# Performance work log

Hardware: AMD Instinct MI355X
Metric: run time of the kernel (lower is better)

The kernel has to match this reference:

```python
import jax, jax.numpy as jnp
from jax import lax
import numpy as np

NEIGHBORS = ((1, 3), (0, 2, 4), (1, 5), (0, 4, 6), (1, 3, 5, 7), (2, 4, 8), (3, 7), (4, 6, 8), (5, 7))
EDGE_SRC = np.array([s for t, ns in enumerate(NEIGHBORS) for s in ns])  # 25 edges
EDGE_DST = np.array([t for t, ns in enumerate(NEIGHBORS) for _ in ns])
NE = len(EDGE_SRC)  # 25
NG, SP = 9, 64      # num_grids, single_plane = 576 // 9
R, C_IN, C_OUT, ROI = 64, 256, 576, 14
GN_GROUPS = 36
EPS = 1e-5


def conv2d(x, w, b, stride, pad):
    y = lax.conv_general_dilated(x, w, (stride, stride), [(pad, pad), (pad, pad)],
                                 dimension_numbers=('NCHW', 'OIHW', 'NCHW'))
    return y + b[None, :, None, None]


def group_norm(x, groups, gamma, beta):
    B, C, H, W = x.shape
    xg = x.reshape(B, groups, -1)
    mu = xg.mean(-1, keepdims=True)
    var = xg.var(-1, keepdims=True)
    xn = ((xg - mu) / jnp.sqrt(var + EPS)).reshape(B, C, H, W)
    return xn * gamma[None, :, None, None] + beta[None, :, None, None]


def edge_conv(inp, dw_w, dw_b, pw_w, pw_b):
    # depthwise 5x5 (groups=SP) then pointwise 1x1
    y = lax.conv_general_dilated(inp, dw_w, (1, 1), [(2, 2), (2, 2)],
                                 dimension_numbers=('NCHW', 'OIHW', 'NCHW'),
                                 feature_group_count=SP) + dw_b[None, :, None, None]
    return jnp.einsum('bchw,oc->bohw', y, pw_w) + pw_b[None, :, None, None]


def deconv_grouped(x, w_t, b, groups):
    # torch ConvTranspose2d(k=4, s=2, p=1, groups) as lhs-dilated conv
    k, s, p = 4, 2, 1
    in_c, out_g = w_t.shape[0], w_t.shape[1]
    in_g = in_c // groups
    w = w_t.reshape(groups, in_g, out_g, k, k).transpose(0, 2, 1, 3, 4).reshape(groups * out_g, in_g, k, k)
    w = jnp.flip(w, (-2, -1))
    y = lax.conv_general_dilated(x, w, (1, 1), [(k - 1 - p, k - 1 - p)] * 2,
                                 lhs_dilation=(s, s),
                                 dimension_numbers=('NCHW', 'OIHW', 'NCHW'),
                                 feature_group_count=groups)
    return y + b[None, :, None, None]


def setup_inputs() -> dict:
    key = jax.random.key(0)
    ks = iter(jax.random.split(key, 32))
    n = lambda shape, s=0.02: jax.random.normal(next(ks), shape, jnp.float32) * s
    inp = {
        'x': jax.random.normal(next(ks), (R, C_IN, ROI, ROI), jnp.float32),
        'convs_w0': n((C_OUT, C_IN, 3, 3)),
        'convs_b0': n((C_OUT,)),
        'convs_w': n((7, C_OUT, C_OUT, 3, 3)),
        'convs_b': n((7, C_OUT)),
        'gn_gamma': jnp.ones((8, C_OUT), jnp.float32),
        'gn_beta': jnp.zeros((8, C_OUT), jnp.float32),
        'fo_dw_w': n((NE, SP, 1, 5, 5), 0.05),
        'fo_dw_b': n((NE, SP)),
        'fo_pw_w': n((NE, SP, SP), 0.05),
        'fo_pw_b': n((NE, SP)),
        'so_dw_w': n((NE, SP, 1, 5, 5), 0.05),
        'so_dw_b': n((NE, SP)),
        'so_pw_w': n((NE, SP, SP), 0.05),
        'so_pw_b': n((NE, SP)),
        'up1_w': n((C_OUT, SP, 4, 4), 0.01),
        'up1_b': jnp.zeros((C_OUT,), jnp.float32),
        'sbn1_gamma': jnp.ones((C_OUT,), jnp.float32),
        'sbn1_beta': jnp.zeros((C_OUT,), jnp.float32),
        'up2_w': n((C_OUT, 1, 4, 4), 0.01),
        'up2_b': jnp.full((NG,), -np.log(0.99 / 0.01), jnp.float32),
    }
    return inp


def reference(x, convs_w0, convs_b0, convs_w, convs_b, gn_gamma, gn_beta,
              fo_dw_w, fo_dw_b, fo_pw_w, fo_pw_b,
              so_dw_w, so_dw_b, so_pw_w, so_pw_b,
              up1_w, up1_b, sbn1_gamma, sbn1_beta, up2_w, up2_b):
    # dense conv stack: stride 2 first, then 7 stride-1 convs (GN + ReLU each)
    h = jax.nn.relu(group_norm(conv2d(x, convs_w0, convs_b0, 2, 1), GN_GROUPS, gn_gamma[0], gn_beta[0]))
    for i in range(7):
        h = jax.nn.relu(group_norm(conv2d(h, convs_w[i], convs_b[i], 1, 1),
                                   GN_GROUPS, gn_gamma[i + 1], gn_beta[i + 1]))
    B, _, Hh, Wh = h.shape  # [B, 576, 7, 7]
    xg = h.reshape(B, NG, SP, Hh, Wh).transpose(1, 0, 2, 3, 4)  # [9, B, 64, 7, 7]
    # first-order message passing over 25 grid edges
    msgs1 = jax.vmap(edge_conv)(xg[EDGE_SRC], fo_dw_w, fo_dw_b, fo_pw_w, fo_pw_b)
    first = xg + jax.ops.segment_sum(msgs1, EDGE_DST, num_segments=NG)
    # second-order message passing (sources are first-order features)
    msgs2 = jax.vmap(edge_conv)(first[EDGE_SRC], so_dw_w, so_dw_b, so_pw_w, so_pw_b)
    second = xg + jax.ops.segment_sum(msgs2, EDGE_DST, num_segments=NG)
    x2 = second.transpose(1, 0, 2, 3, 4).reshape(B, NG * SP, Hh, Wh)

    def head(t):
        t = deconv_grouped(t, up1_w, up1_b, NG)           # [B, 576, 14, 14]
        t = jax.nn.relu(group_norm(t, NG, sbn1_gamma, sbn1_beta))
        return deconv_grouped(t, up2_w, up2_b, NG)        # [B, 9, 28, 28]

    return (head(h), head(x2))
```

## Files before the change

kernel.cpp:

```cpp
#include <hip/hip_runtime.h>
#include <hip/hip_bf16.h>

#define BB 64
#define CIN 256
#define CC 576
#define NGR 9
#define SPC 64
#define HW7 49
#define HW14 196
#define HW28 784

__device__ __constant__ int EDGE_SRC_C[24] = {1,3, 0,2,4, 1,5, 0,4,6, 1,3,5,7, 2,4,8, 3,7, 4,6,8, 5,7};
__device__ __constant__ int EDGE_OFF_C[9]  = {0,2,5,7,10,14,17,19,22};
__device__ __constant__ int EDGE_CNT_C[9]  = {2,3,2,3,4,3,2,3,2};

static __device__ __forceinline__ float bf2f(__hip_bfloat16 v){ return __bfloat162float(v); }
static __device__ __forceinline__ __hip_bfloat16 f2bf(float v){ return __float2bfloat16(v); }
static __device__ __forceinline__ float ldin(const void* p, size_t i, int isbf){
  return isbf ? bf2f(((const __hip_bfloat16*)p)[i]) : ((const float*)p)[i];
}

using bfrag = __attribute__((ext_vector_type(8))) short;
using f32x4 = __attribute__((ext_vector_type(4))) float;

__global__ void detect_kernel(const unsigned short* xs, int* flag) {
  if (threadIdx.x==0 && blockIdx.x==0) {
    int plaus = 0;
    for (int i=0;i<64;i++){
      unsigned short u = xs[2*i];
      int e = (u>>7)&0xFF;
      if (e>=100 && e<=140) plaus++;
    }
    *flag = (plaus >= 40) ? 1 : 0;
  }
}

__global__ __launch_bounds__(256) void xcvt_kernel(
    const void* __restrict__ x, const int* __restrict__ flagp,
    __hip_bfloat16* __restrict__ act0) {
  const int b = blockIdx.x, icb = blockIdx.y, pxb = blockIdx.z, t = threadIdx.x;
  const int isbf = *flagp;
  __shared__ float lds[32][29];
  for (int idx=t; idx<32*28; idx+=256){
    int i = idx/28, j = idx - i*28;
    lds[i][j] = ldin(x, ((size_t)b*CIN + icb*32+i)*HW14 + pxb*28 + j, isbf);
  }
  __syncthreads();
  for (int idx=t; idx<28*32; idx+=256){
    int j = idx >> 5, i = idx & 31;
    act0[((size_t)b*HW14 + pxb*28 + j)*CIN + icb*32 + i] = f2bf(lds[i][j]);
  }
}

__global__ __launch_bounds__(256) void wcvt0_kernel(
    const void* __restrict__ w, const int* __restrict__ flagp,
    __hip_bfloat16* __restrict__ dst) {
  const int oc = blockIdx.x, t = threadIdx.x;
  const int isbf = *flagp;
  __shared__ float lds[2304];
  for (int idx=t; idx<2304; idx+=256)
    lds[idx] = ldin(w, (size_t)oc*2304 + idx, isbf);
  __syncthreads();
  for (int idx=t; idx<2304; idx+=256){
    int koff = idx >> 8, rem = idx & 255;
    int icb = rem >> 5, ici = rem & 31;
    dst[(((size_t)koff*8 + icb)*CC + oc)*32 + ici] = f2bf(lds[rem*9 + koff]);
  }
}

__global__ __launch_bounds__(256) void wcvtL_kernel(
    const void* __restrict__ w, int li, const int* __restrict__ flagp,
    __hip_bfloat16* __restrict__ dst) {
  const int oc = blockIdx.x, t = threadIdx.x;
  const int isbf = *flagp;
  __shared__ float lds[5184];
  for (int idx=t; idx<5184; idx+=256)
    lds[idx] = ldin(w, ((size_t)li*CC + oc)*5184 + idx, isbf);
  __syncthreads();
  for (int idx=t; idx<5184; idx+=256){
    int koff = idx / 576, rem = idx - koff*576;
    int icb = rem >> 5, ici = rem & 31;
    dst[(((size_t)koff*18 + icb)*CC + oc)*32 + ici] = f2bf(lds[rem*9 + koff]);
  }
}

__global__ __launch_bounds__(256) void wcvtAll2_kernel(
    const void* __restrict__ w, const int* __restrict__ flagp,
    __hip_bfloat16* __restrict__ dst_base) {
  const int oc0 = blockIdx.x*2, li = blockIdx.y, t = threadIdx.x;
  const int isbf = *flagp;
  __hip_bfloat16* dst = dst_base + (size_t)li * (9u*18u*576u*32u);
  __shared__ alignas(16) __hip_bfloat16 lds[2*5184];

  if (isbf){
    const unsigned short* ws = (const unsigned short*)w;
    for (int idx=t; idx<1296; idx+=256){
      int ocl = idx/648, j = idx - ocl*648;
      *(bfrag*)(lds + ocl*5184 + j*8) =
        *(const bfrag*)(ws + ((size_t)(li*CC + oc0+ocl))*5184 + j*8);
    }
  } else {
    const float* wf = (const float*)w;
    for (int idx=t; idx<1296; idx+=256){
      int ocl = idx/648, j = idx - ocl*648;
      const float* s = wf + ((size_t)(li*CC + oc0+ocl))*5184 + j*8;
      f32x4 v0 = *(const f32x4*)(s);
      f32x4 v1 = *(const f32x4*)(s+4);
      alignas(16) __hip_bfloat16 tmp[8];
      #pragma unroll
      for (int u=0;u<4;u++){ tmp[u] = f2bf(v0[u]); tmp[4+u] = f2bf(v1[u]); }
      *(bfrag*)(lds + ocl*5184 + j*8) = *(const bfrag*)tmp;
    }
  }
  __syncthreads();

  for (int idx=t; idx<1296; idx+=256){
    int g = idx>>1, ocl = idx&1;
    int koff = g/72, r = g - koff*72;
    int icb = r>>2, q = r&3;
    const __hip_bfloat16* src = lds + ocl*5184;
    alignas(16) __hip_bfloat16 tmp[8];
    #pragma unroll
    for (int u=0;u<8;u++)
      tmp[u] = src[(icb*32 + q*8 + u)*9 + koff];
    *(bfrag*)(dst + (((size_t)koff*18 + icb)*CC + (oc0+ocl))*32 + q*8) =
        *(const bfrag*)tmp;
  }
}

static __device__ __forceinline__ void epilogue_gn(
    float* s_out, float* s_stats, const f32x4 (&acc)[2][2],
    int wm, int wn, int ln, int quad, int t,
    const void* bias, int bias_off,
    const void* gamma, const void* beta, int goff,
    int nbb, int isbf, int b,
    __hip_bfloat16* __restrict__ out)
{
  __syncthreads();
  #pragma unroll
  for (int nf=0; nf<2; nf++){
    int chl = wn*32 + nf*16 + ln;
    float bv = ldin(bias, (size_t)bias_off + nbb + chl, isbf);
    #pragma unroll
    for (int mf=0; mf<2; mf++){
      #pragma unroll
      for (int r=0; r<4; r++){
        int px = wm*32 + mf*16 + quad*4 + r;
        s_out[chl*65 + px] = acc[mf][nf][r] + bv;
      }
    }
  }
  __syncthreads();
  {
    int wv = t >> 6, l = t & 63;
    float s=0.f, ss=0.f;
    for (int j=l; j<784; j+=64){
      int cq = j/49, px = j - cq*49;
      float v = s_out[(wv*16+cq)*65 + px];
      s += v; ss += v*v;
    }
    #pragma unroll
    for (int o=32;o>0;o>>=1){ s+=__shfl_down(s,o); ss+=__shfl_down(ss,o); }
    if (l==0){
      float mean=s/784.f, var=ss/784.f-mean*mean;
      s_stats[wv*2]=mean; s_stats[wv*2+1]=rsqrtf(fmaxf(var,0.f)+1e-5f);
    }
  }
  __syncthreads();
  for (int idx=t; idx<392; idx+=256){
    int px = idx>>3, ck = idx&7;
    alignas(16) __hip_bfloat16 tmp[8];
    #pragma unroll
    for (int u=0;u<8;u++){
      int chl = ck*8+u;
      int gi = chl>>4;
      float ga = ldin(gamma, (size_t)goff + nbb + chl, isbf);
      float be = ldin(beta,  (size_t)goff + nbb + chl, isbf);
      float v = (s_out[chl*65+px]-s_stats[gi*2])*s_stats[gi*2+1]*ga + be;
      tmp[u] = f2bf(fmaxf(v,0.f));
    }
    *(bfrag*)(out + ((size_t)b*64+px)*CC + nbb + ck*8) = *(const bfrag*)tmp;
  }
}

__global__ __launch_bounds__(256) void conv3_v6_kernel(
    const __hip_bfloat16* __restrict__ A,
    const __hip_bfloat16* __restrict__ Wb,
    const void* __restrict__ bias, int bias_off,
    const void* __restrict__ gamma, const void* __restrict__ beta, int goff,
    const int* __restrict__ flagp,
    __hip_bfloat16* __restrict__ out) {
  const int t = threadIdx.x;
  const int l = t & 63, w = t >> 6;
  const int wm = w & 1, wn = (w >> 1) & 1;
  const int ln = l & 15, quad = l >> 4;
  const int b = blockIdx.x, nbb = blockIdx.y*32;
  const int isbf = *flagp;

  __shared__ alignas(16) char smem[14400];
  __shared__ float s_stats[4];
  __hip_bfloat16* sA0 = (__hip_bfloat16*)smem;
  __hip_bfloat16* sA1 = (__hip_bfloat16*)(smem + 7200);
  float* s_out = (float*)smem;

  if (t < 16){
    bfrag z = {0,0,0,0,0,0,0,0};
    __hip_bfloat16* sb = (t<8)? sA0 : sA1;
    *(bfrag*)(sb + 49*72 + (t&7)*8) = z;
  }

  int r0a[9], r1a[9];
  {
    int p0 = wm*32 + ln, p1 = p0+16;
    int y0=p0/7, x0=p0-y0*7, y1=p1/7, x1=p1-y1*7;
    bool v0=p0<49, v1=p1<49;
    #pragma unroll
    for (int koff=0;koff<9;koff++){
      int dy=koff/3-1, dx=koff-(koff/3)*3-1;
      int sy0=y0+dy,sx0=x0+dx, sy1=y1+dy,sx1=x1+dx;
      r0a[koff] = (v0&&sy0>=0&&sy0<7&&sx0>=0&&sx0<7)? sy0*7+sx0 : 49;
      r1a[koff] = (v1&&sy1>=0&&sy1<7&&sx1>=0&&sx1<7)? sy1*7+sx1 : 49;
    }
  }

  f32x4 acc2[2];
  acc2[0] = (f32x4){0.f,0.f,0.f,0.f};
  acc2[1] = (f32x4){0.f,0.f,0.f,0.f};

  const int i0r = t>>3, is8 = (t&7)*8;
  const int i1r = i0r + 32;
  const bool has1 = (t < 136);
  const __hip_bfloat16* Ab = A + (size_t)b*64*CC;

  *(bfrag*)(sA0 + i0r*72 + is8) = *(const bfrag*)(Ab + (size_t)i0r*CC + is8);
  if (has1)
    *(bfrag*)(sA0 + i1r*72 + is8) = *(const bfrag*)(Ab + (size_t)i1r*CC + is8);
  __syncthreads();

  const int nidx = nbb + wn*16 + ln;
  const __hip_bfloat16* wbase = Wb + (size_t)nidx*32 + quad*8;
  for (int c=0; c<9; c++){
    __hip_bfloat16* curb = (c&1)? sA1 : sA0;
    bfrag rs0, rs1;
    const bool pf = (c<8);
    if (pf){
      rs0 = *(const bfrag*)(Ab + (size_t)i0r*CC + (c+1)*64 + is8);
      if (has1) rs1 = *(const bfrag*)(Ab + (size_t)i1r*CC + (c+1)*64 + is8);
    }
    #pragma unroll
    for (int koff=0;koff<9;koff++){
      const int ra0 = r0a[koff]*72 + quad*8;
      const int ra1 = r1a[koff]*72 + quad*8;
      #pragma unroll
      for (int ks=0; ks<2; ks++){
        const __hip_bfloat16* wp = wbase + (size_t)(koff*18 + c*2 + ks)*18432;
        bfrag b0 = *(const bfrag*)(wp);
        bfrag a0 = *(const bfrag*)(curb + ra0 + ks*32);
        bfrag a1 = *(const bfrag*)(curb + ra1 + ks*32);
        acc2[0] = __builtin_amdgcn_mfma_f32_16x16x32_bf16(a0, b0, acc2[0], 0,0,0);
        acc2[1] = __builtin_amdgcn_mfma_f32_16x16x32_bf16(a1, b0, acc2[1], 0,0,0);
      }
    }
    if (pf){
      __hip_bfloat16* nxtb = (c&1)? sA0 : sA1;
      *(bfrag*)(nxtb + i0r*72 + is8) = rs0;
      if (has1) *(bfrag*)(nxtb + i1r*72 + is8) = rs1;
    }
    __syncthreads();
  }

  {
    const int chl = wn*16 + ln;
    float bv = ldin(bias, (size_t)bias_off + nbb + chl, isbf);
    #pragma unroll
    for (int mf=0; mf<2; mf++)
      #pragma unroll
      for (int r=0;r<4;r++){
        int px = wm*32 + mf*16 + quad*4 + r;
        s_out[chl*65 + px] = acc2[mf][r] + bv;
      }
  }
  __syncthreads();
  {
    int wv = t >> 6, l2 = t & 63;
    if (wv < 2){
      float s=0.f, ss=0.f;
      for (int j=l2; j<784; j+=64){
        int cq = j/49, px = j - cq*49;
        float v = s_out[(wv*16+cq)*65 + px];
        s += v; ss += v*v;
      }
      #pragma unroll
      for (int o=32;o>0;o>>=1){ s+=__shfl_down(s,o); ss+=__shfl_down(ss,o); }
      if (l2==0){
        float mean=s/784.f, var=ss/784.f-mean*mean;
        s_stats[wv*2]=mean; s_stats[wv*2+1]=rsqrtf(fmaxf(var,0.f)+1e-5f);
      }
    }
  }
  __syncthreads();
  if (t < 196){
    int px = t>>2, ck = t&3;
    alignas(16) __hip_bfloat16 tmp[8];
    #pragma unroll
    for (int u=0;u<8;u++){
      int chl = ck*8+u;
      int gi = chl>>4;
      float ga = ldin(gamma, (size_t)goff + nbb + chl, isbf);
      float be = ldin(beta,  (size_t)goff + nbb + chl, isbf);
      float v = (s_out[chl*65+px]-s_stats[gi*2])*s_stats[gi*2+1]*ga + be;
      tmp[u] = f2bf(fmaxf(v,0.f));
    }
    *(bfrag*)(out + ((size_t)b*64+px)*CC + nbb + ck*8) = *(const bfrag*)tmp;
  }
}

__global__ __launch_bounds__(256) void conv0_fused_kernel(
    const __hip_bfloat16* __restrict__ A,
    const __hip_bfloat16* __restrict__ Wb,
    const void* __restrict__ bias,
    const void* __restrict__ gamma, const void* __restrict__ beta,
    const int* __restrict__ flagp,
    __hip_bfloat16* __restrict__ out) {
  const int t = threadIdx.x;
  const int l = t & 63, w = t >> 6;
  const int wm = w & 1, wn = w >> 1;
  const int ln = l & 15, quad = l >> 4;
  const int b = blockIdx.x, nbb = blockIdx.y*64;

  __shared__ alignas(16) __hip_bfloat16 sC[197*40];
  __shared__ alignas(16) float s_out_arr[64*65];
  __shared__ float s_stats[8];

  if (t < 4){
    bfrag z = {0,0,0,0,0,0,0,0};
    *(bfrag*)(sC + 196*40 + t*8) = z;
  }

  int yy[2], xx[2]; bool pv[2];
  #pragma unroll
  for (int mf=0; mf<2; mf++){
    int p = wm*32 + mf*16 + ln;
    pv[mf] = p<49; yy[mf]=p/7; xx[mf]=p-yy[mf]*7;
  }

  f32x4 acc[2][2];
  #pragma unroll
  for (int i=0;i<2;i++)
    #pragma unroll
    for (int j=0;j<2;j++) acc[i][j] = (f32x4){0.f,0.f,0.f,0.f};

  for (int icb=0; icb<8; icb++){
    __syncthreads();
    for (int idx=t*8; idx<6272; idx+=2048){
      int px = idx>>5, ic = idx&31;
      *(bfrag*)(sC + px*40 + ic) = *(const bfrag*)(A + ((size_t)b*196+px)*256 + icb*32 + ic);
    }
    __syncthreads();
    for (int koff=0; koff<9; koff++){
      const int dy = koff/3 - 1, dx = koff - (koff/3)*3 - 1;
      int sy0=2*yy[0]+dy, sx0=2*xx[0]+dx;
      int r0 = (pv[0]&&sy0>=0&&sy0<14&&sx0>=0&&sx0<14) ? sy0*14+sx0 : 196;
      int sy1=2*yy[1]+dy, sx1=2*xx[1]+dx;
      int r1 = (pv[1]&&sy1>=0&&sy1<14&&sx1>=0&&sx1<14) ? sy1*14+sx1 : 196;
      bfrag a0 = *(const bfrag*)(sC + r0*40 + quad*8);
      bfrag a1 = *(const bfrag*)(sC + r1*40 + quad*8);
      const __hip_bfloat16* wp = Wb + ((size_t)(koff*8+icb)*576 + nbb + wn*32 + ln)*32 + quad*8;
      bfrag b0 = *(const bfrag*)(wp);
      bfrag b1 = *(const bfrag*)(wp + 16*32);
      acc[0][0] = __builtin_amdgcn_mfma_f32_16x16x32_bf16(a0, b0, acc[0][0], 0,0,0);
      acc[1][0] = __builtin_amdgcn_mfma_f32_16x16x32_bf16(a1, b0, acc[1][0], 0,0,0);
      acc[0][1] = __builtin_amdgcn_mfma_f32_16x16x32_bf16(a0, b1, acc[0][1], 0,0,0);
      acc[1][1] = __builtin_amdgcn_mfma_f32_16x16x32_bf16(a1, b1, acc[1][1], 0,0,0);
    }
  }

  epilogue_gn(s_out_arr, s_stats, acc, wm, wn, ln, quad, t,
              bias, 0, gamma, beta, 0, nbb, *flagp, b, out);
}

__global__ __launch_bounds__(256) void dw_edge_kernel(
    const __hip_bfloat16* __restrict__ F,
    const void* __restrict__ dw_w,
    const void* __restrict__ dw_b,
    const int* __restrict__ flagp,
    __hip_bfloat16* __restrict__ Y) {
  const int b = blockIdx.x, e = blockIdx.y, t = threadIdx.x;
  const int isbf = *flagp;
  const int src = EDGE_SRC_C[e];
  __shared__ alignas(16) __hip_bfloat16 sA[50*72];
  for (int idx=t; idx<400; idx+=256){
    if (idx < 392){
      int px = idx>>3, ic = (idx&7)*8;
      *(bfrag*)(sA + px*72 + ic) = *(const bfrag*)(F + ((size_t)b*64+px)*CC + src*64 + ic);
    } else {
      bfrag z = {0,0,0,0,0,0,0,0};
      *(bfrag*)(sA + 49*72 + (idx-392)*8) = z;
    }
  }
  __syncthreads();
  const int ch = t & 63, wv = t >> 6;
  float wd[25];
  #pragma unroll
  for (int j=0;j<25;j++) wd[j] = ldin(dw_w, (size_t)e*1600 + ch*25 + j, isbf);
  float dwb = ldin(dw_b, e*64 + ch, isbf);
  for (int px=wv; px<49; px+=4){
    int oy=px/7, ox=px-oy*7;
    float a = dwb;
    #pragma unroll
    for (int u=0;u<5;u++){
      int py = oy+u-2;
      bool vy = (py>=0)&&(py<7);
      #pragma unroll
      for (int v=0;v<5;v++){
        int pxx = ox+v-2;
        int r = (vy && pxx>=0 && pxx<7) ? py*7+pxx : 49;
        a += bf2f(sA[r*72 + ch]) * wd[u*5+v];
      }
    }
    Y[((size_t)(e*64+b)*49 + px)*64 + ch] = f2bf(a);
  }
}

__global__ __launch_bounds__(256) void pwpack_kernel(
    const void* __restrict__ pw_fo, const void* __restrict__ pw_so,
    const int* __restrict__ flagp,
    __hip_bfloat16* __restrict__ dfo, __hip_bfloat16* __restrict__ dso) {
  const int e = blockIdx.x, t = threadIdx.x;
  const int isbf = *flagp;
  for (int idx=t; idx<4096; idx+=256){
    dfo[(size_t)e*4096+idx] = f2bf(ldin(pw_fo, (size_t)e*4096+idx, isbf));
    dso[(size_t)e*4096+idx] = f2bf(ldin(pw_so, (size_t)e*4096+idx, isbf));
  }
}

__global__ __launch_bounds__(256) void pw_seg_kernel(
    const __hip_bfloat16* __restrict__ Y,
    const __hip_bfloat16* __restrict__ base,
    const __hip_bfloat16* __restrict__ pwb,
    const void* __restrict__ pw_b,
    const int* __restrict__ flagp,
    __hip_bfloat16* __restrict__ out) {
  const int t = threadIdx.x, l = t & 63, w = t >> 6;
  const int wm = w & 1, wn = w >> 1;
  const int ln = l & 15, quad = l >> 4;
  const int dst = blockIdx.y;
  const int mt = blockIdx.x*64 + wm*32;
  const int m0 = mt + ln, m1 = m0 + 16;

  f32x4 acc[2][2];
  #pragma unroll
  for (int i=0;i<2;i++)
    #pragma unroll
    for (int j=0;j<2;j++) acc[i][j] = (f32x4){0.f,0.f,0.f,0.f};

  const int eoff = EDGE_OFF_C[dst], ecnt = EDGE_CNT_C[dst];
  for (int k=0;k<ecnt;k++){
    const __hip_bfloat16* Ye = Y + (size_t)(eoff+k)*3136*64;
    const __hip_bfloat16* pe = pwb + (size_t)(eoff+k)*4096;
    #pragma unroll
    for (int ks=0; ks<2; ks++){
      const int kq = ks*32 + quad*8;
      bfrag a0 = *(const bfrag*)(Ye + (size_t)m0*64 + kq);
      bfrag a1 = *(const bfrag*)(Ye + (size_t)m1*64 + kq);
      bfrag b0 = *(const bfrag*)(pe + (wn*32+ln)*64 + kq);
      bfrag b1 = *(const bfrag*)(pe + (wn*32+ln+16)*64 + kq);
      acc[0][0] = __builtin_amdgcn_mfma_f32_16x16x32_bf16(a0, b0, acc[0][0], 0,0,0);
      acc[1][0] = __builtin_amdgcn_mfma_f32_16x16x32_bf16(a1, b0, acc[1][0], 0,0,0);
      acc[0][1] = __builtin_amdgcn_mfma_f32_16x16x32_bf16(a0, b1, acc[0][1], 0,0,0);
      acc[1][1] = __builtin_amdgcn_mfma_f32_16x16x32_bf16(a1, b1, acc[1][1], 0,0,0);
    }
  }

  const int isbf = *flagp;
  #pragma unroll
  for (int nf=0; nf<2; nf++){
    int n = wn*32 + nf*16 + ln;
    float pbs = 0.f;
    for (int k=0;k<ecnt;k++) pbs += ldin(pw_b, (size_t)(eoff+k)*64 + n, isbf);
    #pragma unroll
    for (int mf=0; mf<2; mf++){
      #pragma unroll
      for (int r=0; r<4; r++){
        int m = mt + mf*16 + quad*4 + r;
        int bb = m/49, px = m - bb*49;
        size_t oi = ((size_t)bb*64 + px)*CC + dst*64 + n;
        out[oi] = f2bf(bf2f(base[oi]) + acc[mf][nf][r] + pbs);
      }
    }
  }
}

__global__ __launch_bounds__(256) void wpack_dc1_kernel(
    const void* __restrict__ w1, const int* __restrict__ flagp,
    __hip_bfloat16* __restrict__ dst) {
  const int gtap = blockIdx.x, t = threadIdx.x;
  const int isbf = *flagp;
  const int g = gtap >> 4, tap = gtap & 15;
  for (int idx=t; idx<64*64; idx+=256){
    int oc = idx >> 6, ic = idx & 63;
    dst[((size_t)gtap*64 + oc)*64 + ic] =
        f2bf(ldin(w1, ((size_t)(g*64+ic)*64 + oc)*16 + tap, isbf));
  }
}

__global__ __launch_bounds__(256) void dc1_cls_kernel(
    const __hip_bfloat16* __restrict__ H,
    const __hip_bfloat16* __restrict__ Wp,
    const void* __restrict__ b1,
    const int* __restrict__ flagp,
    __hip_bfloat16* __restrict__ mid) {
  const int t = threadIdx.x;
  const int l = t & 63, w = t >> 6;
  const int wm = w & 1, wn = w >> 1;
  const int ln = l & 15, quad = l >> 4;
  const int Mt = blockIdx.x;
  const int cls = blockIdx.y;
  const int g = blockIdx.z;
  const int ry = cls >> 1, rx = cls & 1;
  const int b0 = (Mt*64)/49;

  __shared__ alignas(16) __hip_bfloat16 sX[3*50*72];

  {
    const bfrag z = {0,0,0,0,0,0,0,0};
    for (int idx=t; idx<1200; idx+=256){
      int bi = idx/400, rem = idx - bi*400;
      int p = rem>>3, ch = (rem&7)*8;
      bfrag v = z;
      if (p < 49 && (b0+bi) < 64)
        v = *(const bfrag*)(H + ((size_t)((b0+bi)*64) + p)*CC + g*64 + ch);
      *(bfrag*)(sX + (bi*50+p)*72 + ch) = v;
    }
  }

  int aoff[2][4];
  #pragma unroll
  for (int mf=0; mf<2; mf++){
    int m = Mt*64 + wm*32 + mf*16 + ln;
    int b = m/49, p = m - b*49;
    int py = p/7, pxx = p - py*7;
    int bloc = b - b0;
    #pragma unroll
    for (int kyi=0;kyi<2;kyi++){
      int iy = py + ry - kyi;
      bool vy = (iy>=0)&&(iy<7);
      #pragma unroll
      for (int kxi=0;kxi<2;kxi++){
        int ix = pxx + rx - kxi;
        int r = (vy && ix>=0 && ix<7) ? iy*7+ix : 49;
        aoff[mf][kyi*2+kxi] = (bloc*50 + r)*72 + quad*8;
      }
    }
  }

  f32x4 acc[2][2];
  #pragma unroll
  for (int i=0;i<2;i++)
    #pragma unroll
    for (int j=0;j<2;j++) acc[i][j] = (f32x4){0.f,0.f,0.f,0.f};

  __syncthreads();

  const int ky0 = 1-ry, kx0 = 1-rx;
  #pragma unroll
  for (int kyi=0;kyi<2;kyi++){
    #pragma unroll
    for (int kxi=0;kxi<2;kxi++){
      const int tap = (ky0+2*kyi)*4 + (kx0+2*kxi);
      const __hip_bfloat16* wb =
          Wp + ((size_t)(g*16+tap)*64 + wn*32 + ln)*64 + quad*8;
      const int ao0 = aoff[0][kyi*2+kxi], ao1 = aoff[1][kyi*2+kxi];
      #pragma unroll
      for (int half=0; half<2; half++){
        bfrag a0 = *(const bfrag*)(sX + ao0 + half*32);
        bfrag a1 = *(const bfrag*)(sX + ao1 + half*32);
        bfrag w0 = *(const bfrag*)(wb + half*32);
        bfrag w1 = *(const bfrag*)(wb + 16*64 + half*32);
        acc[0][0] = __builtin_amdgcn_mfma_f32_16x16x32_bf16(a0, w0, acc[0][0], 0,0,0);
        acc[1][0] = __builtin_amdgcn_mfma_f32_16x16x32_bf16(a1, w0, acc[1][0], 0,0,0);
        acc[0][1] = __builtin_amdgcn_mfma_f32_16x16x32_bf16(a0, w1, acc[0][1], 0,0,0);
        acc[1][1] = __builtin_amdgcn_mfma_f32_16x16x32_bf16(a1, w1, acc[1][1], 0,0,0);
      }
    }
  }

  const int isbf = *flagp;
  size_t ob[2][4];
  #pragma unroll
  for (int mf=0;mf<2;mf++){
    #pragma unroll
    for (int r=0;r<4;r++){
      int m = Mt*64 + wm*32 + mf*16 + quad*4 + r;
      int b = m/49, p = m - b*49;
      int py = p/7, pxx = p - py*7;
      int oy = 2*py + ry, ox = 2*pxx + rx;
      ob[mf][r] = ((size_t)b*196 + oy*14 + ox)*CC + g*64;
    }
  }
  #pragma unroll
  for (int nf=0;nf<2;nf++){
    int n = wn*32 + nf*16 + ln;
    float bv = ldin(b1, g*64 + n, isbf);
    #pragma unroll
    for (int mf=0;mf<2;mf++){
      #pragma unroll
      for (int r=0;r<4;r++)
        mid[ob[mf][r] + n] = f2bf(acc[mf][nf][r] + bv);
    }
  }
}

__global__ __launch_bounds__(256) void dc2gn_kernel(
    const __hip_bfloat16* __restrict__ mid,
    const void* __restrict__ gamma, const void* __restrict__ beta,
    const void* __restrict__ w2,
    const void* __restrict__ b2,
    const int* __restrict__ flagp,
    void* __restrict__ outp,
    size_t out_elem_off) {
  const int isbf = *flagp;
  const int b=blockIdx.x, g=blockIdx.y, z=blockIdx.z, t=threadIdx.x;
  const int c = t & 63;
  __shared__ __hip_bfloat16 s_mid[64*113];
  __shared__ float s_w2[64][17];
  __shared__ float red[8]; __shared__ float stats[2];
  const __hip_bfloat16* mbase = mid + (size_t)b*196*CC + g*64;

  {
    float s=0.f, ss=0.f;
    for (int idx=t; idx<12544; idx+=256){
      int ipx = idx>>6;
      float v = bf2f(mbase[(size_t)ipx*CC + (idx&63)]);
      s+=v; ss+=v*v;
    }
    #pragma unroll
    for (int o=32;o>0;o>>=1){ s+=__shfl_down(s,o); ss+=__shfl_down(ss,o); }
    int wid=t>>6;
    if ((t&63)==0){ red[wid]=s; red[4+wid]=ss; }
  }
  for (int idx=t; idx<1024; idx+=256)
    s_w2[idx>>4][idx&15] = ldin(w2, (g*SPC + (idx>>4))*16 + (idx&15), isbf);
  __syncthreads();
  if (t==0){
    float S=red[0]+red[1]+red[2]+red[3];
    float SS=red[4]+red[5]+red[6]+red[7];
    float mean=S/12544.f, var=SS/12544.f-mean*mean;
    stats[0]=mean; stats[1]=rsqrtf(fmaxf(var,0.f)+1e-5f);
  }
  __syncthreads();
  const float mean=stats[0], inv=stats[1];
  const int rbase = z*6;
  {
    float ga = ldin(gamma, g*SPC+c, isbf), be = ldin(beta, g*SPC+c, isbf);
    for (int idx=t; idx<7168; idx+=256){
      int pl = idx>>6;
      int ipx = (rbase + pl/14)*14 + (pl%14);
      float v = (bf2f(mbase[(size_t)ipx*CC + c])-mean)*inv*ga + be;
      s_mid[c*113 + pl] = f2bf(fmaxf(v, 0.f));
    }
  }
  __syncthreads();
  float b2v = ldin(b2, g, isbf);
  for (int p=t; p<392; p+=256){
    int oyl = p/28, ox = p - oyl*28;
    int oy = z*14 + oyl;
    float a = b2v;
    for (int cc=0; cc<64; cc++){
      #pragma unroll
      for (int kyi=0;kyi<2;kyi++){
        int ky=((oy+1)&1)+2*kyi; int ny=oy+1-ky;
        if (ny>=0){
          int iy=ny>>1;
          if (iy<14){
            int li = iy - rbase;
            #pragma unroll
            for (int kxi=0;kxi<2;kxi++){
              int kx=((ox+1)&1)+2*kxi; int nx=ox+1-kx;
              if (nx>=0){
                int ix=nx>>1;
                if (ix<14) a += bf2f(s_mid[cc*113 + li*14 + ix])*s_w2[cc][ky*4+kx];
              }
            }
          }
        }
      }
    }
    size_t oidx = out_elem_off + ((size_t)b*NGR+g)*HW28 + oy*28 + ox;
    if (isbf) ((__hip_bfloat16*)outp)[oidx] = f2bf(a);
    else      ((float*)outp)[oidx] = a;
  }
}

extern "C" void kernel_launch(void* const* d_in, const int* in_sizes, int n_in,
                              void* d_out, int out_size, void* d_ws, size_t ws_size,
                              hipStream_t stream) {
  const void* x        = d_in[0];
  const void* convs_w0 = d_in[1];
  const void* convs_b0 = d_in[2];
  const void* convs_w  = d_in[3];
  const void* convs_b  = d_in[4];
  const void* gn_gamma = d_in[5];
  const void* gn_beta  = d_in[6];
  const void* fo_dw_w  = d_in[7];
  const void* fo_dw_b  = d_in[8];
  const void* fo_pw_w  = d_in[9];
  const void* fo_pw_b  = d_in[10];
  const void* so_dw_w  = d_in[11];
  const void* so_dw_b  = d_in[12];
  const void* so_pw_w  = d_in[13];
  const void* so_pw_b  = d_in[14];
  const void* up1_w    = d_in[15];
  const void* up1_b    = d_in[16];
  const void* sbn_g    = d_in[17];
  const void* sbn_b    = d_in[18];
  const void* up2_w    = d_in[19];
  const void* up2_b    = d_in[20];
  (void)in_sizes; (void)n_in; (void)out_size;

  int* flag = (int*)d_ws;
  char* wsb = (char*)d_ws + 16;
  __hip_bfloat16* act0   = (__hip_bfloat16*)(wsb);
  __hip_bfloat16* wbuf   = (__hip_bfloat16*)(wsb + 6422528);
  __hip_bfloat16* actA   = (__hip_bfloat16*)(wsb + 12394496);
  __hip_bfloat16* actB   = (__hip_bfloat16*)(wsb + 17113088);
  __hip_bfloat16* bufF   = (__hip_bfloat16*)(wsb + 21831680);
  __hip_bfloat16* secN   = (__hip_bfloat16*)(wsb + 26550272);
  __hip_bfloat16* wpack  = (__hip_bfloat16*)(wsb + 31268864);
  __hip_bfloat16* pwbF   = (__hip_bfloat16*)(wsb + 32448512);
  __hip_bfloat16* pwbS   = (__hip_bfloat16*)(wsb + 32645120);
  __hip_bfloat16* Y      = (__hip_bfloat16*)(wsb);
  __hip_bfloat16* mid    = (__hip_bfloat16*)(wsb);

  const size_t WL_ELEMS = (size_t)9*18*576*32;
  const size_t wall_off = 33u*1024u*1024u;
  const bool bigws = ws_size >= 16 + wall_off + 7*WL_ELEMS*sizeof(__hip_bfloat16);
  __hip_bfloat16* wall = (__hip_bfloat16*)(wsb + wall_off);

  detect_kernel<<<1, 1, 0, stream>>>((const unsigned short*)x, flag);

  if (bigws)
    wcvtAll2_kernel<<<dim3(288,7), 256, 0, stream>>>(convs_w, flag, wall);

  xcvt_kernel<<<dim3(BB,8,7), 256, 0, stream>>>(x, flag, act0);
  wcvt0_kernel<<<CC, 256, 0, stream>>>(convs_w0, flag, wbuf);
  conv0_fused_kernel<<<dim3(64,9), 256, 0, stream>>>(
      act0, wbuf, convs_b0, gn_gamma, gn_beta, flag, actA);

  __hip_bfloat16* cur = actA; __hip_bfloat16* nxt = actB;
  for (int i=0;i<7;i++){
    const __hip_bfloat16* wb_i;
    if (bigws){
      wb_i = wall + (size_t)i*WL_ELEMS;
    } else {
      wcvtL_kernel<<<CC, 256, 0, stream>>>(convs_w, i, flag, wbuf);
      wb_i = wbuf;
    }
    conv3_v6_kernel<<<dim3(64,18), 256, 0, stream>>>(
        cur, wb_i, convs_b, i*CC, gn_gamma, gn_beta, (i+1)*CC, flag, nxt);
    __hip_bfloat16* tmp=cur; cur=nxt; nxt=tmp;
  }

  wpack_dc1_kernel<<<144, 256, 0, stream>>>(up1_w, flag, wpack);
  pwpack_kernel<<<24, 256, 0, stream>>>(fo_pw_w, so_pw_w, flag, pwbF, pwbS);

  dw_edge_kernel<<<dim3(BB,24), 256, 0, stream>>>(cur, fo_dw_w, fo_dw_b, flag, Y);
  pw_seg_kernel<<<dim3(49,NGR), 256, 0, stream>>>(Y, cur, pwbF, fo_pw_b, flag, bufF);
  dw_edge_kernel<<<dim3(BB,24), 256, 0, stream>>>(bufF, so_dw_w, so_dw_b, flag, Y);
  pw_seg_kernel<<<dim3(49,NGR), 256, 0, stream>>>(Y, cur, pwbS, so_pw_b, flag, secN);

  dc1_cls_kernel<<<dim3(49,4,NGR), 256, 0, stream>>>(cur, wpack, up1_b, flag, mid);
  dc2gn_kernel<<<dim3(BB,NGR,2), 256, 0, stream>>>(mid, sbn_g, sbn_b, up2_w, up2_b, flag, d_out, 0);
  dc1_cls_kernel<<<dim3(49,4,NGR), 256, 0, stream>>>(secN, wpack, up1_b, flag, mid);
  dc2gn_kernel<<<dim3(BB,NGR,2), 256, 0, stream>>>(mid, sbn_g, sbn_b, up2_w, up2_b, flag, d_out, (size_t)BB*NGR*HW28);
}
```

Measured before the change: 871.0 us.

## Split 3x3 conv blocks to one GN group with 2 waves and swizzled grid

The 3x3 conv+GroupNorm kernel now uses 128-thread blocks, each computing 16 output channels (one GN group) for one ROI, which doubles the grid to 2304 blocks. A swizzled block index spreads neighbouring blocks across channel slices and ROIs, aiming at better L2 reuse of weights or activations and more parallelism. Each block still stages the full 49x64 activation tile, so activation loads and LDS traffic per output channel double, and fewer waves are available per block to hide latency.

```diff
diff --git a/kernel.cpp b/kernel.cpp
--- a/kernel.cpp
+++ b/kernel.cpp
@@ -183,7 +183,7 @@
   }
 }
 
-__global__ __launch_bounds__(256) void conv3_v6_kernel(
+__global__ __launch_bounds__(128) void conv3_v7_kernel(
     const __hip_bfloat16* __restrict__ A,
     const __hip_bfloat16* __restrict__ Wb,
     const void* __restrict__ bias, int bias_off,
@@ -191,14 +191,16 @@
     const int* __restrict__ flagp,
     __hip_bfloat16* __restrict__ out) {
   const int t = threadIdx.x;
-  const int l = t & 63, w = t >> 6;
-  const int wm = w & 1, wn = (w >> 1) & 1;
+  const int l = t & 63, wm = t >> 6;
   const int ln = l & 15, quad = l >> 4;
-  const int b = blockIdx.x, nbb = blockIdx.y*32;
+  const int id = blockIdx.x;
+  const int sw = (id & 7)*288 + (id >> 3);
+  const int b = sw & 63, slice = sw >> 6;
+  const int nbb = slice*16;
   const int isbf = *flagp;
 
   __shared__ alignas(16) char smem[14400];
-  __shared__ float s_stats[4];
+  __shared__ float s_stats[2];
   __hip_bfloat16* sA0 = (__hip_bfloat16*)smem;
   __hip_bfloat16* sA1 = (__hip_bfloat16*)(smem + 7200);
   float* s_out = (float*)smem;
@@ -227,25 +229,30 @@
   acc2[0] = (f32x4){0.f,0.f,0.f,0.f};
   acc2[1] = (f32x4){0.f,0.f,0.f,0.f};
 
-  const int i0r = t>>3, is8 = (t&7)*8;
-  const int i1r = i0r + 32;
-  const bool has1 = (t < 136);
+  const bool has2 = (t < 136), has3 = (t < 8);
+  const int s0r = t>>3,        s0c = (t&7)*8;
+  const int s1r = (t+128)>>3,  s1c = s0c;
+  const int s2r = (t+256)>>3,  s2c = s0c;
+  const int s3r = 48,          s3c = t*8;
   const __hip_bfloat16* Ab = A + (size_t)b*64*CC;
 
-  *(bfrag*)(sA0 + i0r*72 + is8) = *(const bfrag*)(Ab + (size_t)i0r*CC + is8);
-  if (has1)
-    *(bfrag*)(sA0 + i1r*72 + is8) = *(const bfrag*)(Ab + (size_t)i1r*CC + is8);
-  __syncthreads();
-
-  const int nidx = nbb + wn*16 + ln;
-  const __hip_bfloat16* wbase = Wb + (size_t)nidx*32 + quad*8;
+  *(bfrag*)(sA0 + s0r*72 + s0c) = *(const bfrag*)(Ab + (size_t)s0r*CC + s0c);
+  *(bfrag*)(sA0 + s1r*72 + s1c) = *(const bfrag*)(Ab + (size_t)s1r*CC + s1c);
+  if (has2) *(bfrag*)(sA0 + s2r*72 + s2c) = *(const bfrag*)(Ab + (size_t)s2r*CC + s2c);
+  if (has3) *(bfrag*)(sA0 + s3r*72 + s3c) = *(const bfrag*)(Ab + (size_t)s3r*CC + s3c);
+  __syncthreads();
+
+  const __hip_bfloat16* wbase = Wb + (size_t)(nbb + ln)*32 + quad*8;
   for (int c=0; c<9; c++){
     __hip_bfloat16* curb = (c&1)? sA1 : sA0;
-    bfrag rs0, rs1;
+    bfrag rs0, rs1, rs2, rs3;
     const bool pf = (c<8);
     if (pf){
-      rs0 = *(const bfrag*)(Ab + (size_t)i0r*CC + (c+1)*64 + is8);
-      if (has1) rs1 = *(const bfrag*)(Ab + (size_t)i1r*CC + (c+1)*64 + is8);
+      const int co = (c+1)*64;
+      rs0 = *(const bfrag*)(Ab + (size_t)s0r*CC + co + s0c);
+      rs1 = *(const bfrag*)(Ab + (size_t)s1r*CC + co + s1c);
+      if (has2) rs2 = *(const bfrag*)(Ab + (size_t)s2r*CC + co + s2c);
+      if (has3) rs3 = *(const bfrag*)(Ab + (size_t)s3r*CC + co + s3c);
     }
     #pragma unroll
     for (int koff=0;koff<9;koff++){
@@ -263,14 +270,16 @@
     }
     if (pf){
       __hip_bfloat16* nxtb = (c&1)? sA0 : sA1;
-      *(bfrag*)(nxtb + i0r*72 + is8) = rs0;
-      if (has1) *(bfrag*)(nxtb + i1r*72 + is8) = rs1;
+      *(bfrag*)(nxtb + s0r*72 + s0c) = rs0;
+      *(bfrag*)(nxtb + s1r*72 + s1c) = rs1;
+      if (has2) *(bfrag*)(nxtb + s2r*72 + s2c) = rs2;
+      if (has3) *(bfrag*)(nxtb + s3r*72 + s3c) = rs3;
     }
     __syncthreads();
   }
 
   {
-    const int chl = wn*16 + ln;
+    const int chl = ln;
     float bv = ldin(bias, (size_t)bias_off + nbb + chl, isbf);
     #pragma unroll
     for (int mf=0; mf<2; mf++)
@@ -281,34 +290,31 @@
       }
   }
   __syncthreads();
-  {
-    int wv = t >> 6, l2 = t & 63;
-    if (wv < 2){
-      float s=0.f, ss=0.f;
-      for (int j=l2; j<784; j+=64){
-        int cq = j/49, px = j - cq*49;
-        float v = s_out[(wv*16+cq)*65 + px];
-        s += v; ss += v*v;
-      }
-      #pragma unroll
-      for (int o=32;o>0;o>>=1){ s+=__shfl_down(s,o); ss+=__shfl_down(ss,o); }
-      if (l2==0){
-        float mean=s/784.f, var=ss/784.f-mean*mean;
-        s_stats[wv*2]=mean; s_stats[wv*2+1]=rsqrtf(fmaxf(var,0.f)+1e-5f);
-      }
-    }
-  }
-  __syncthreads();
-  if (t < 196){
-    int px = t>>2, ck = t&3;
+  if (t < 64){
+    float s=0.f, ss=0.f;
+    for (int j=t; j<784; j+=64){
+      int cq = j/49, px = j - cq*49;
+      float v = s_out[cq*65 + px];
+      s += v; ss += v*v;
+    }
+    #pragma unroll
+    for (int o=32;o>0;o>>=1){ s+=__shfl_down(s,o); ss+=__shfl_down(ss,o); }
+    if (t==0){
+      float mean=s/784.f, var=ss/784.f-mean*mean;
+      s_stats[0]=mean; s_stats[1]=rsqrtf(fmaxf(var,0.f)+1e-5f);
+    }
+  }
+  __syncthreads();
+  if (t < 98){
+    int px = t>>1, ck = t&1;
+    const float mean = s_stats[0], inv = s_stats[1];
     alignas(16) __hip_bfloat16 tmp[8];
     #pragma unroll
     for (int u=0;u<8;u++){
       int chl = ck*8+u;
-      int gi = chl>>4;
       float ga = ldin(gamma, (size_t)goff + nbb + chl, isbf);
       float be = ldin(beta,  (size_t)goff + nbb + chl, isbf);
-      float v = (s_out[chl*65+px]-s_stats[gi*2])*s_stats[gi*2+1]*ga + be;
+      float v = (s_out[chl*65+px]-mean)*inv*ga + be;
       tmp[u] = f2bf(fmaxf(v,0.f));
     }
     *(bfrag*)(out + ((size_t)b*64+px)*CC + nbb + ck*8) = *(const bfrag*)tmp;
@@ -756,7 +762,7 @@
       wcvtL_kernel<<<CC, 256, 0, stream>>>(convs_w, i, flag, wbuf);
       wb_i = wbuf;
     }
-    conv3_v6_kernel<<<dim3(64,18), 256, 0, stream>>>(
+    conv3_v7_kernel<<<2304, 128, 0, stream>>>(
         cur, wb_i, convs_b, i*CC, gn_gamma, gn_beta, (i+1)*CC, flag, nxt);
     __hip_bfloat16* tmp=cur; cur=nxt; nxt=tmp;
   }
```

Result: slower. 936.1 us (+7.5%).
